# Optimization experiments

Measured on AMD Instinct MI355X. Metric: run time of the kernel, lower is better.

The kernel has to match this reference:

```python
import math
import jax, jax.numpy as jnp
import numpy as np

B, T, S, H, L, NH = 2, 512, 2048, 768, 32, 12
INTERMED = 4 * H


def _make_pe(max_len, hidden):
    position = np.arange(max_len)[:, None].astype(np.float32)
    div_term = np.exp(np.arange(0, hidden, 2).astype(np.float32) * (-math.log(10000.0) / hidden))
    pe = np.zeros((max_len, hidden), dtype=np.float32)
    pe[:, 0::2] = np.sin(position * div_term)
    pe[:, 1::2] = np.cos(position * div_term)
    return jnp.asarray(pe)


def setup_inputs() -> dict:
    key = jax.random.key(0)
    ks = jax.random.split(key, 10)
    token_reps = jax.random.normal(ks[0], (B, T, H), dtype=jnp.float32)
    starts = jax.random.randint(ks[1], (B, S), 0, T - L)
    lens = jax.random.randint(ks[2], (B, S), 1, L + 1)
    span_ids = jnp.stack([starts, starts + lens], axis=-1)  # (B,S,2)
    span_masks = jax.random.uniform(ks[3], (B, S)) > 0.2
    pe = _make_pe(T, H)
    dummy_query = jax.random.normal(ks[4], (H,), dtype=jnp.float32) * 0.02
    in_proj_w = jax.random.normal(ks[5], (3 * H, H), dtype=jnp.float32) * 0.02
    in_proj_b = jnp.zeros((3 * H,), jnp.float32)
    out_proj_w = jax.random.normal(ks[6], (H, H), dtype=jnp.float32) * 0.02
    out_proj_b = jnp.zeros((H,), jnp.float32)
    norm_g = jnp.ones((H,), jnp.float32)
    norm_b = jnp.zeros((H,), jnp.float32)
    ffn_w1 = jax.random.normal(ks[7], (INTERMED, H), dtype=jnp.float32) * (math.sqrt(2.0 / H))
    ffn_b1 = jnp.zeros((INTERMED,), jnp.float32)
    ffn_w2 = jax.random.normal(ks[8], (H, INTERMED), dtype=jnp.float32) * (math.sqrt(2.0 / INTERMED))
    ffn_b2 = jnp.zeros((H,), jnp.float32)
    return dict(token_reps=token_reps, span_ids=span_ids, span_masks=span_masks,
                pooling=0, pe=pe, dummy_query=dummy_query,
                in_proj_w=in_proj_w, in_proj_b=in_proj_b,
                out_proj_w=out_proj_w, out_proj_b=out_proj_b,
                norm_g=norm_g, norm_b=norm_b,
                ffn_w1=ffn_w1, ffn_b1=ffn_b1, ffn_w2=ffn_w2, ffn_b2=ffn_b2)


def _layernorm(x, g, b, eps=1e-5):
    mu = jnp.mean(x, axis=-1, keepdims=True)
    var = jnp.mean(jnp.square(x - mu), axis=-1, keepdims=True)
    return (x - mu) * jax.lax.rsqrt(var + eps) * g + b


def reference(token_reps, span_ids, span_masks, pooling, pe, dummy_query,
              in_proj_w, in_proj_b, out_proj_w, out_proj_b,
              norm_g, norm_b, ffn_w1, ffn_b1, ffn_w2, ffn_b2):
    b, t, h = token_reps.shape
    s = span_ids.shape[1]
    hd = h // NH
    # positional encoding over the sequence (dropout=0 / eval mode)
    x = token_reps + pe[:t]
    # ragged -> padded gather of span tokens
    starts = span_ids[..., 0]
    lens = (span_ids[..., 1] - starts) * span_masks.astype(span_ids.dtype)  # (B,S)
    ar = jnp.arange(L)
    pos = starts[..., None] + ar                     # (B,S,L)
    valid = ar[None, None, :] < lens[..., None]      # (B,S,L) True = real token
    idx = jnp.clip(pos, 0, t - 1)
    gathered = jax.vmap(lambda xb, ib: xb[ib])(x, idx)   # (B,S,L,H)
    gathered = gathered * valid[..., None]
    # guard fully-masked rows (masked-out / zero-len spans): keep one key valid,
    # output is zeroed at the end anyway (matches torch span_reps[~mask]=0)
    any_v = jnp.any(valid, axis=-1)
    valid = valid.at[..., 0].set(valid[..., 0] | ~any_v)
    # single-query multi-head attention (torch nn.MultiheadAttention math)
    Wq, Wk, Wv = jnp.split(in_proj_w, 3, axis=0)
    bq, bk, bv = jnp.split(in_proj_b, 3, axis=0)
    q = (dummy_query @ Wq.T + bq).reshape(NH, hd)                  # (NH,hd)
    k = (gathered @ Wk.T + bk).reshape(b, s, L, NH, hd)
    v = (gathered @ Wv.T + bv).reshape(b, s, L, NH, hd)
    scores = jnp.einsum('nd,bslnd->bsnl', q, k) / math.sqrt(hd)    # (B,S,NH,L)
    scores = jnp.where(valid[:, :, None, :], scores, -jnp.inf)
    attn = jax.nn.softmax(scores, axis=-1)
    ctx = jnp.einsum('bsnl,bslnd->bsnd', attn, v).reshape(b, s, h)
    attn_out = ctx @ out_proj_w.T + out_proj_b
    # residual + LayerNorm, FFN, residual + same LayerNorm
    x1 = _layernorm(attn_out + dummy_query, norm_g, norm_b)
    ffn = jax.nn.relu(x1 @ ffn_w1.T + ffn_b1) @ ffn_w2.T + ffn_b2
    out = _layernorm(ffn + x1, norm_g, norm_b)
    out = out * span_masks[..., None]
    return out
```

## Files before the change

kernel.cpp:

```cpp
#include <hip/hip_runtime.h>
#include <math.h>

static constexpr int B_  = 2;
static constexpr int T_  = 512;
static constexpr int S_  = 2048;
static constexpr int H_  = 768;
static constexpr int L_  = 32;
static constexpr int NH_ = 12;
static constexpr int HD_ = 64;
static constexpr int IM_ = 3072;

typedef __bf16 bf16x8 __attribute__((ext_vector_type(8)));
typedef float  f32x4  __attribute__((ext_vector_type(4)));

__device__ __forceinline__ float bf2f(unsigned short u) {
    return __uint_as_float(((unsigned)u) << 16);
}
__device__ __forceinline__ unsigned short f2bf(float f) {
    unsigned u = __float_as_uint(f);
    u += 0x7fffu + ((u >> 16) & 1u);
    return (unsigned short)(u >> 16);
}
__device__ __forceinline__ void gl_lds16(const void* g, void* l) {
    __builtin_amdgcn_global_load_lds((const __attribute__((address_space(1))) void*)g,
                                     (__attribute__((address_space(3))) void*)l, 16, 0, 0);
}

__global__ void k_q(const float* __restrict__ dq, const float* __restrict__ w,
                    const float* __restrict__ b, float* __restrict__ q,
                    const int* __restrict__ raw, int* __restrict__ mout) {
    int wv = threadIdx.x >> 6, lane = threadIdx.x & 63;
    int i = blockIdx.x * 4 + wv;
    const float* row = w + (size_t)i * H_;
    float acc = 0.f;
#pragma unroll
    for (int k = 0; k < 12; ++k) acc += dq[lane + 64 * k] * row[lane + 64 * k];
    for (int m = 32; m; m >>= 1) acc += __shfl_xor(acc, m, 64);
    if (lane == 0) q[i] = acc + b[i];
    if (blockIdx.x == 0) {
        __shared__ int bad;
        if (threadIdx.x == 0) bad = 0;
        __syncthreads();
        for (int t = threadIdx.x; t < 1024; t += 256) {
            int v = raw[t];
            if (v != 0 && v != 1) bad = 1;
        }
        __syncthreads();
        int byte_layout = bad;
        const unsigned char* rb = (const unsigned char*)raw;
        for (int t = threadIdx.x; t < B_ * S_; t += 256)
            mout[t] = byte_layout ? (int)rb[t] : raw[t];
    }
}

static constexpr int CWB = 2880;
__global__ void k_castw(const float* __restrict__ s0, const float* __restrict__ s1,
                        const float* __restrict__ s2, const float* __restrict__ s3,
                        unsigned short* __restrict__ d0, unsigned short* __restrict__ d1,
                        unsigned short* __restrict__ d2, unsigned short* __restrict__ d3,
                        const float* __restrict__ q, const float* __restrict__ wk,
                        float* __restrict__ wq) {
    if (blockIdx.x >= CWB) {
        int i = (blockIdx.x - CWB) * 256 + threadIdx.x;
        int n = i / H_, hh = i % H_;
        float acc = 0.f;
        for (int d = 0; d < HD_; ++d)
            acc += q[n * HD_ + d] * wk[(size_t)(H_ + n * HD_ + d) * H_ + hh];
        wq[i] = acc;
        return;
    }
    const long n0 = (long)H_ * H_, n2 = (long)IM_ * H_;
    long gid = (long)(blockIdx.x * 256 + threadIdx.x) * 8;
    const float* s; unsigned short* d; long off;
    if (gid < n0)                { s = s0; d = d0; off = gid; }
    else if (gid < 2 * n0)       { s = s1; d = d1; off = gid - n0; }
    else if (gid < 2 * n0 + n2)  { s = s2; d = d2; off = gid - 2 * n0; }
    else                         { s = s3; d = d3; off = gid - 2 * n0 - n2; }
    float4 f0 = *(const float4*)(s + off);
    float4 f1 = *(const float4*)(s + off + 4);
    uint4 o;
    o.x = (unsigned)f2bf(f0.x) | ((unsigned)f2bf(f0.y) << 16);
    o.y = (unsigned)f2bf(f0.z) | ((unsigned)f2bf(f0.w) << 16);
    o.z = (unsigned)f2bf(f1.x) | ((unsigned)f2bf(f1.y) << 16);
    o.w = (unsigned)f2bf(f1.z) | ((unsigned)f2bf(f1.w) << 16);
    *(uint4*)(d + off) = o;
}

__global__ void k_xstok(const float* __restrict__ tr, const float* __restrict__ pe,
                        const float* __restrict__ wq,
                        unsigned short* __restrict__ xbf, float* __restrict__ stok) {
    __shared__ float sx[H_];
    int bt = blockIdx.x, tid = threadIdx.x;
    const float* trow = tr + (size_t)bt * H_;
    const float* prow = pe + (size_t)(bt % T_) * H_;
    if (tid < 192) {
        int h0 = tid * 4;
        float4 a = *(const float4*)(trow + h0);
        float4 p = *(const float4*)(prow + h0);
        float v0 = a.x + p.x, v1 = a.y + p.y, v2 = a.z + p.z, v3 = a.w + p.w;
        sx[h0] = v0; sx[h0 + 1] = v1; sx[h0 + 2] = v2; sx[h0 + 3] = v3;
        uint2 o;
        o.x = (unsigned)f2bf(v0) | ((unsigned)f2bf(v1) << 16);
        o.y = (unsigned)f2bf(v2) | ((unsigned)f2bf(v3) << 16);
        *(uint2*)(xbf + (size_t)bt * H_ + h0) = o;
    }
    __syncthreads();
    int lane = tid & 63, w = tid >> 6;
    float xv[12];
#pragma unroll
    for (int k = 0; k < 12; ++k) xv[k] = sx[lane + 64 * k];
#pragma unroll
    for (int hh = 0; hh < 3; ++hh) {
        int n = w * 3 + hh;
        const float* wr = wq + (size_t)n * H_;
        float acc = 0.f;
#pragma unroll
        for (int k = 0; k < 12; ++k) acc += xv[k] * wr[lane + 64 * k];
        for (int m = 32; m; m >>= 1) acc += __shfl_xor(acc, m, 64);
        if (lane == 0) stok[bt * NH_ + n] = acc;
    }
}

__global__ void k_castv4(const unsigned short* __restrict__ p, size_t pstr,
                         unsigned short* __restrict__ dst, int n) {
    int i = (blockIdx.x * 256 + threadIdx.x) * 8;
    if (i >= n) return;
    float a[8] = {};
#pragma unroll
    for (int z = 0; z < 4; ++z) {
        uint4 u = *(const uint4*)(p + z * pstr + i);
        a[0] += bf2f((unsigned short)(u.x & 0xffff));
        a[1] += bf2f((unsigned short)(u.x >> 16));
        a[2] += bf2f((unsigned short)(u.y & 0xffff));
        a[3] += bf2f((unsigned short)(u.y >> 16));
        a[4] += bf2f((unsigned short)(u.z & 0xffff));
        a[5] += bf2f((unsigned short)(u.z >> 16));
        a[6] += bf2f((unsigned short)(u.w & 0xffff));
        a[7] += bf2f((unsigned short)(u.w >> 16));
    }
    uint4 o;
    o.x = (unsigned)f2bf(a[0]) | ((unsigned)f2bf(a[1]) << 16);
    o.y = (unsigned)f2bf(a[2]) | ((unsigned)f2bf(a[3]) << 16);
    o.z = (unsigned)f2bf(a[4]) | ((unsigned)f2bf(a[5]) << 16);
    o.w = (unsigned)f2bf(a[6]) | ((unsigned)f2bf(a[7]) << 16);
    *(uint4*)(dst + i) = o;
}

#define STG3(b_, k0e_) do {                                                   \
    unsigned short* _la = AsB + (b_) * 4096 + wid * 1024;                     \
    unsigned short* _lb = BsB + (b_) * 4096 + wid * 1024;                     \
    gl_lds16(agp + (k0e_), _la);                                              \
    gl_lds16(agp + (size_t)16 * K + (k0e_), _la + 512);                       \
    gl_lds16(bgp + (k0e_), _lb);                                              \
    gl_lds16(bgp + (size_t)16 * K + (k0e_), _lb + 512);                       \
} while (0)

template <bool RELU, bool SPLIT>
__device__ __forceinline__
void gemm_d3_body(const unsigned short* __restrict__ A, const unsigned short* __restrict__ W,
                  const float* __restrict__ bias, unsigned short* __restrict__ Cout,
                  int M, int N, int K, int kLen, int TX, int SP) {
    __shared__ unsigned short As[3][4096];
    __shared__ unsigned short Bs[3][4096];
    unsigned short* const AsB = &As[0][0];
    unsigned short* const BsB = &Bs[0][0];
    const int qx = blockIdx.x & 7, t = blockIdx.x >> 3;
    const int gi = t / TX, x = t - gi * TX;
    const int g = gi * 8 + qx;
    int y, z;
    if (SPLIT) { y = g / SP; z = g - y * SP; } else { y = g; z = 0; }
    const int bm = y * 128, bn = x * 128;
    const int kOff = z * kLen;

    const int tid = threadIdx.x, lane = tid & 63, wid = tid >> 6;
    const int wm = (wid >> 1) * 64, wn = (wid & 1) * 64;
    const int r16 = lane >> 2, c4 = lane & 3;
    const int swc = (c4 ^ ((r16 >> 1) & 3)) * 8;
    const unsigned short* agp = A + (size_t)(bm + wid * 32 + r16) * K + kOff + swc;
    const unsigned short* bgp = W + (size_t)(bn + wid * 32 + r16) * K + kOff + swc;

    f32x4 acc[4][4];
#pragma unroll
    for (int i = 0; i < 4; ++i)
#pragma unroll
        for (int j = 0; j < 4; ++j) acc[i][j] = f32x4{0.f, 0.f, 0.f, 0.f};

    const int mrow = lane & 15;
    const int q4 = lane >> 4;
    const int sw = (q4 ^ ((mrow >> 1) & 3)) * 8;
    const int NIT = kLen >> 5;

    STG3(0, 0);
    STG3(1, 1 << 5);
    int c0 = 0, c1 = 1, c2 = 2;
    for (int it = 0; it < NIT; ++it) {
        int nk = it + 2; if (nk > NIT - 1) nk = NIT - 1;
        STG3(c2, nk << 5);
        asm volatile("s_waitcnt vmcnt(8)" ::: "memory");
        __builtin_amdgcn_s_barrier();
        __builtin_amdgcn_sched_barrier(0);
        const unsigned short* Ac = AsB + c0 * 4096;
        const unsigned short* Bc = BsB + c0 * 4096;
        bf16x8 af[4], bfr[4];
#pragma unroll
        for (int i = 0; i < 4; ++i)
            af[i] = *(const bf16x8*)(Ac + (wm + i * 16 + mrow) * 32 + sw);
#pragma unroll
        for (int j = 0; j < 4; ++j)
            bfr[j] = *(const bf16x8*)(Bc + (wn + j * 16 + mrow) * 32 + sw);
        asm volatile("s_waitcnt lgkmcnt(0)" ::: "memory");
        __builtin_amdgcn_sched_barrier(0);
#pragma unroll
        for (int i = 0; i < 4; ++i)
#pragma unroll
            for (int j = 0; j < 4; ++j)
                acc[i][j] = __builtin_amdgcn_mfma_f32_16x16x32_bf16(af[i], bfr[j], acc[i][j], 0, 0, 0);
        __builtin_amdgcn_s_barrier();
        __builtin_amdgcn_sched_barrier(0);
        int tmp = c0; c0 = c1; c1 = c2; c2 = tmp;
    }
    asm volatile("s_waitcnt vmcnt(0)" ::: "memory");

    const bool addb = !SPLIT || z == 0;
    unsigned short* outp = SPLIT ? Cout + (size_t)z * M * N : Cout;
    const int lr = (lane >> 4) * 4, lc = lane & 15;
#pragma unroll
    for (int j = 0; j < 4; ++j) {
        int col = bn + wn + j * 16 + lc;
        float bv = addb ? bias[col] : 0.f;
#pragma unroll
        for (int i = 0; i < 4; ++i) {
            int row0 = bm + wm + i * 16 + lr;
#pragma unroll
            for (int r = 0; r < 4; ++r) {
                float v = acc[i][j][r] + bv;
                if (RELU) v = fmaxf(v, 0.f);
                outp[(size_t)(row0 + r) * N + col] = f2bf(v);
            }
        }
    }
}

__global__ __launch_bounds__(256)
void g3_vtok(const unsigned short* A, const unsigned short* W, const float* bias,
             unsigned short* Cout, int M, int N, int K, int kLen, int TX, int SP) {
    gemm_d3_body<false, true>(A, W, bias, Cout, M, N, K, kLen, TX, SP);
}
__global__ __launch_bounds__(256)
void g3_oproj(const unsigned short* A, const unsigned short* W, const float* bias,
              unsigned short* Cout, int M, int N, int K, int kLen, int TX, int SP) {
    gemm_d3_body<false, true>(A, W, bias, Cout, M, N, K, kLen, TX, SP);
}
__global__ __launch_bounds__(256)
void g3_ffn1(const unsigned short* A, const unsigned short* W, const float* bias,
             unsigned short* Cout, int M, int N, int K, int kLen, int TX, int SP) {
    gemm_d3_body<true, false>(A, W, bias, Cout, M, N, K, kLen, TX, SP);
}
__global__ __launch_bounds__(256)
void g3_ffn2(const unsigned short* A, const unsigned short* W, const float* bias,
             unsigned short* Cout, int M, int N, int K, int kLen, int TX, int SP) {
    gemm_d3_body<false, true>(A, W, bias, Cout, M, N, K, kLen, TX, SP);
}

__global__ void k_attn(const float* __restrict__ stok, const unsigned short* __restrict__ vtok,
                       const int* __restrict__ span_ids, const int* __restrict__ masks,
                       unsigned short* __restrict__ ctx) {
    int r = blockIdx.x, b = r / S_;
    unsigned short* out = ctx + (size_t)r * H_;
    int tid = threadIdx.x;
    __shared__ float w[NH_][L_];
    __shared__ int idxs[L_];
    __shared__ int s_len;
    if (tid == 0) {
        int m = masks[r];
        int st = span_ids[2 * r], en = span_ids[2 * r + 1];
        int len = m ? (en - st) : 0;
        len = len < 0 ? 0 : (len > L_ ? L_ : len);
        s_len = len;
    }
    __syncthreads();
    int len = s_len;
    if (len == 0) {
        for (int h2 = tid; h2 < H_ / 2; h2 += 256) ((unsigned*)out)[h2] = 0u;
        return;
    }
    if (tid < L_) {
        int p = span_ids[2 * r] + tid;
        idxs[tid] = p < 0 ? 0 : (p > T_ - 1 ? T_ - 1 : p);
    }
    __syncthreads();
    for (int i = tid; i < NH_ * L_; i += 256) {
        int n = i / L_, l = i % L_;
        w[n][l] = (l < len) ? stok[(size_t)(b * T_ + idxs[l]) * NH_ + n] * 0.125f : -INFINITY;
    }
    __syncthreads();
    if (tid < NH_) {
        float mx = -INFINITY;
        for (int l = 0; l < len; ++l) mx = fmaxf(mx, w[tid][l]);
        float sum = 0.f;
        for (int l = 0; l < len; ++l) { float e = __expf(w[tid][l] - mx); w[tid][l] = e; sum += e; }
        float inv = 1.f / sum;
        for (int l = 0; l < len; ++l) w[tid][l] *= inv;
    }
    __syncthreads();
    if (tid < 192) {
        int h0 = tid * 4, n = h0 >> 6;
        float a0 = 0.f, a1 = 0.f, a2 = 0.f, a3 = 0.f;
        for (int l = 0; l < len; ++l) {
            float wl = w[n][l];
            const unsigned short* vr = vtok + (size_t)(b * T_ + idxs[l]) * H_ + h0;
            uint2 u = *(const uint2*)vr;
            a0 += wl * bf2f((unsigned short)(u.x & 0xffff));
            a1 += wl * bf2f((unsigned short)(u.x >> 16));
            a2 += wl * bf2f((unsigned short)(u.y & 0xffff));
            a3 += wl * bf2f((unsigned short)(u.y >> 16));
        }
        uint2 o;
        o.x = (unsigned)f2bf(a0) | ((unsigned)f2bf(a1) << 16);
        o.y = (unsigned)f2bf(a2) | ((unsigned)f2bf(a3) << 16);
        *(uint2*)(out + h0) = o;
    }
}

template <bool RESROW, bool MASKOUT, int ZN>
__global__ void k_ln(const unsigned short* __restrict__ parts, size_t pstr,
                     const float* __restrict__ resf, const unsigned short* __restrict__ resb,
                     const float* __restrict__ g, const float* __restrict__ bt,
                     float* __restrict__ outf, unsigned short* __restrict__ outb,
                     const int* __restrict__ masks) {
    int r = blockIdx.x;
    int tid = threadIdx.x;
    float v[3];
    float lsum = 0.f;
#pragma unroll
    for (int i = 0; i < 3; ++i) {
        int h = tid + 256 * i;
        float s = RESROW ? bf2f(resb[(size_t)r * H_ + h]) : resf[h];
#pragma unroll
        for (int z = 0; z < ZN; ++z)
            s += bf2f(parts[z * pstr + (size_t)r * H_ + h]);
        v[i] = s;
        lsum += s;
    }
    __shared__ float sh[256];
    sh[tid] = lsum;
    __syncthreads();
    for (int st = 128; st > 0; st >>= 1) {
        if (tid < st) sh[tid] += sh[tid + st];
        __syncthreads();
    }
    float mean = sh[0] * (1.f / H_);
    __syncthreads();
    float lvar = 0.f;
#pragma unroll
    for (int i = 0; i < 3; ++i) { float d = v[i] - mean; lvar += d * d; }
    sh[tid] = lvar;
    __syncthreads();
    for (int st = 128; st > 0; st >>= 1) {
        if (tid < st) sh[tid] += sh[tid + st];
        __syncthreads();
    }
    float var = sh[0] * (1.f / H_);
    float scale = rsqrtf(var + 1e-5f);
    float mfac = 1.f;
    if (MASKOUT) mfac = masks[r] ? 1.f : 0.f;
#pragma unroll
    for (int i = 0; i < 3; ++i) {
        int h = tid + 256 * i;
        float o = ((v[i] - mean) * scale * g[h] + bt[h]) * mfac;
        if (MASKOUT) outf[(size_t)r * H_ + h] = o;
        else         outb[(size_t)r * H_ + h] = f2bf(o);
    }
}

extern "C" void kernel_launch(void* const* d_in, const int* in_sizes, int n_in,
                              void* d_out, int out_size, void* d_ws, size_t ws_size,
                              hipStream_t stream) {
    const float* token_reps = (const float*)d_in[0];
    const int*   span_ids   = (const int*)d_in[1];
    const int*   masks_raw  = (const int*)d_in[2];
    const float* pe   = (const float*)d_in[4];
    const float* dq   = (const float*)d_in[5];
    const float* in_w = (const float*)d_in[6];
    const float* in_b = (const float*)d_in[7];
    const float* ow   = (const float*)d_in[8];
    const float* ob   = (const float*)d_in[9];
    const float* g    = (const float*)d_in[10];
    const float* bt   = (const float*)d_in[11];
    const float* w1   = (const float*)d_in[12];
    const float* b1   = (const float*)d_in[13];
    const float* w2   = (const float*)d_in[14];
    const float* b2   = (const float*)d_in[15];

    const int BS = B_ * S_;
    const int BT = B_ * T_;

    float* fws   = (float*)d_ws;
    float* stok  = fws;
    float* qv    = stok + BT * NH_;
    float* wqeff = qv + H_;
    unsigned short* us = (unsigned short*)(wqeff + NH_ * H_);
    unsigned short* pbuf = us;
    unsigned short* xbf  = pbuf + (size_t)4 * BS * H_;
    unsigned short* vtok = xbf + (size_t)BT * H_;
    unsigned short* ctx  = vtok + (size_t)BT * H_;
    unsigned short* x1bf = ctx + (size_t)BS * H_;
    unsigned short* f1   = x1bf + (size_t)BS * H_;
    unsigned short* wvb  = f1 + (size_t)BS * IM_;
    unsigned short* owb  = wvb + H_ * H_;
    unsigned short* w1b  = owb + H_ * H_;
    unsigned short* w2b  = w1b + IM_ * H_;
    int* maskn = (int*)(w2b + H_ * IM_);

    k_q<<<H_ / 4, 256, 0, stream>>>(dq, in_w, in_b, qv, masks_raw, maskn);
    k_castw<<<CWB + 36, 256, 0, stream>>>(
        in_w + (size_t)2 * H_ * H_, ow, w1, w2, wvb, owb, w1b, w2b,
        qv, in_w, wqeff);
    k_xstok<<<BT, 256, 0, stream>>>(token_reps, pe, wqeff, xbf, stok);
    g3_vtok<<<192, 256, 0, stream>>>(
        xbf, wvb, in_b + 2 * H_, pbuf, BT, H_, H_, H_ / 4, 6, 4);
    k_castv4<<<(BT * H_ / 8 + 255) / 256, 256, 0, stream>>>(
        pbuf, (size_t)BT * H_, vtok, BT * H_);
    k_attn<<<BS, 256, 0, stream>>>(stok, vtok, span_ids, maskn, ctx);
    g3_oproj<<<384, 256, 0, stream>>>(
        ctx, owb, ob, pbuf, BS, H_, H_, H_ / 2, 6, 2);
    k_ln<false, false, 2><<<BS, 256, 0, stream>>>(
        pbuf, (size_t)BS * H_, dq, nullptr, g, bt, nullptr, x1bf, nullptr);
    g3_ffn1<<<768, 256, 0, stream>>>(
        x1bf, w1b, b1, f1, BS, IM_, H_, H_, 24, 1);
    g3_ffn2<<<384, 256, 0, stream>>>(
        f1, w2b, b2, pbuf, BS, H_, IM_, IM_ / 2, 6, 2);
    k_ln<true, true, 2><<<BS, 256, 0, stream>>>(
        pbuf, (size_t)BS * H_, nullptr, x1bf, g, bt, (float*)d_out, nullptr, maskn);
}
```

Before: 241.4 us.

## Fuse q projection into weight-cast kernel and split-K reduction into attention

```diff
diff --git a/kernel.cpp b/kernel.cpp
--- a/kernel.cpp
+++ b/kernel.cpp
@@ -26,51 +26,54 @@
                                      (__attribute__((address_space(3))) void*)l, 16, 0, 0);
 }
 
-__global__ void k_q(const float* __restrict__ dq, const float* __restrict__ w,
-                    const float* __restrict__ b, float* __restrict__ q,
-                    const int* __restrict__ raw, int* __restrict__ mout) {
-    int wv = threadIdx.x >> 6, lane = threadIdx.x & 63;
-    int i = blockIdx.x * 4 + wv;
-    const float* row = w + (size_t)i * H_;
-    float acc = 0.f;
-#pragma unroll
-    for (int k = 0; k < 12; ++k) acc += dq[lane + 64 * k] * row[lane + 64 * k];
-    for (int m = 32; m; m >>= 1) acc += __shfl_xor(acc, m, 64);
-    if (lane == 0) q[i] = acc + b[i];
-    if (blockIdx.x == 0) {
-        __shared__ int bad;
-        if (threadIdx.x == 0) bad = 0;
+static constexpr int CWB = 2880;
+__global__ void k_castw2(const float* __restrict__ s0, const float* __restrict__ s1,
+                         const float* __restrict__ s2, const float* __restrict__ s3,
+                         unsigned short* __restrict__ d0, unsigned short* __restrict__ d1,
+                         unsigned short* __restrict__ d2, unsigned short* __restrict__ d3,
+                         const float* __restrict__ dq, const float* __restrict__ in_w,
+                         const float* __restrict__ in_b, float* __restrict__ wq,
+                         const int* __restrict__ raw, int* __restrict__ mout) {
+    __shared__ float sq[64];
+    __shared__ int bad;
+    const int tid = threadIdx.x;
+    if (blockIdx.x >= CWB + 36) {
+        if (tid == 0) bad = 0;
         __syncthreads();
-        for (int t = threadIdx.x; t < 1024; t += 256) {
+        for (int t = tid; t < 1024; t += 256) {
             int v = raw[t];
             if (v != 0 && v != 1) bad = 1;
         }
         __syncthreads();
-        int byte_layout = bad;
+        int byl = bad;
         const unsigned char* rb = (const unsigned char*)raw;
-        for (int t = threadIdx.x; t < B_ * S_; t += 256)
-            mout[t] = byte_layout ? (int)rb[t] : raw[t];
-    }
-}
-
-static constexpr int CWB = 2880;
-__global__ void k_castw(const float* __restrict__ s0, const float* __restrict__ s1,
-                        const float* __restrict__ s2, const float* __restrict__ s3,
-                        unsigned short* __restrict__ d0, unsigned short* __restrict__ d1,
-                        unsigned short* __restrict__ d2, unsigned short* __restrict__ d3,
-                        const float* __restrict__ q, const float* __restrict__ wk,
-                        float* __restrict__ wq) {
+        int base = (blockIdx.x - (CWB + 36)) * 1024;
+#pragma unroll
+        for (int k = 0; k < 4; ++k) {
+            int t = base + k * 256 + tid;
+            mout[t] = byl ? (int)rb[t] : raw[t];
+        }
+        return;
+    }
     if (blockIdx.x >= CWB) {
-        int i = (blockIdx.x - CWB) * 256 + threadIdx.x;
-        int n = i / H_, hh = i % H_;
+        int wvb = blockIdx.x - CWB;
+        int n = wvb / 3, seg = wvb - n * 3;
+        if (tid < 64) {
+            const float* row = in_w + (size_t)(n * HD_ + tid) * H_;
+            float acc = 0.f;
+            for (int k = 0; k < H_; ++k) acc += dq[k] * row[k];
+            sq[tid] = acc + in_b[n * HD_ + tid];
+        }
+        __syncthreads();
+        int hh = seg * 256 + tid;
         float acc = 0.f;
         for (int d = 0; d < HD_; ++d)
-            acc += q[n * HD_ + d] * wk[(size_t)(H_ + n * HD_ + d) * H_ + hh];
-        wq[i] = acc;
+            acc += sq[d] * in_w[(size_t)(H_ + n * HD_ + d) * H_ + hh];
+        wq[n * H_ + hh] = acc;
         return;
     }
     const long n0 = (long)H_ * H_, n2 = (long)IM_ * H_;
-    long gid = (long)(blockIdx.x * 256 + threadIdx.x) * 8;
+    long gid = (long)(blockIdx.x * 256 + tid) * 8;
     const float* s; unsigned short* d; long off;
     if (gid < n0)                { s = s0; d = d0; off = gid; }
     else if (gid < 2 * n0)       { s = s1; d = d1; off = gid - n0; }
@@ -121,31 +124,6 @@
     }
 }
 
-__global__ void k_castv4(const unsigned short* __restrict__ p, size_t pstr,
-                         unsigned short* __restrict__ dst, int n) {
-    int i = (blockIdx.x * 256 + threadIdx.x) * 8;
-    if (i >= n) return;
-    float a[8] = {};
-#pragma unroll
-    for (int z = 0; z < 4; ++z) {
-        uint4 u = *(const uint4*)(p + z * pstr + i);
-        a[0] += bf2f((unsigned short)(u.x & 0xffff));
-        a[1] += bf2f((unsigned short)(u.x >> 16));
-        a[2] += bf2f((unsigned short)(u.y & 0xffff));
-        a[3] += bf2f((unsigned short)(u.y >> 16));
-        a[4] += bf2f((unsigned short)(u.z & 0xffff));
-        a[5] += bf2f((unsigned short)(u.z >> 16));
-        a[6] += bf2f((unsigned short)(u.w & 0xffff));
-        a[7] += bf2f((unsigned short)(u.w >> 16));
-    }
-    uint4 o;
-    o.x = (unsigned)f2bf(a[0]) | ((unsigned)f2bf(a[1]) << 16);
-    o.y = (unsigned)f2bf(a[2]) | ((unsigned)f2bf(a[3]) << 16);
-    o.z = (unsigned)f2bf(a[4]) | ((unsigned)f2bf(a[5]) << 16);
-    o.w = (unsigned)f2bf(a[6]) | ((unsigned)f2bf(a[7]) << 16);
-    *(uint4*)(dst + i) = o;
-}
-
 #define STG3(b_, k0e_) do {                                                   \
     unsigned short* _la = AsB + (b_) * 4096 + wid * 1024;                     \
     unsigned short* _lb = BsB + (b_) * 4096 + wid * 1024;                     \
@@ -262,9 +240,9 @@
     gemm_d3_body<false, true>(A, W, bias, Cout, M, N, K, kLen, TX, SP);
 }
 
-__global__ void k_attn(const float* __restrict__ stok, const unsigned short* __restrict__ vtok,
-                       const int* __restrict__ span_ids, const int* __restrict__ masks,
-                       unsigned short* __restrict__ ctx) {
+__global__ void k_attn4(const float* __restrict__ stok, const unsigned short* __restrict__ pbuf,
+                        size_t pstr, const int* __restrict__ span_ids,
+                        const int* __restrict__ masks, unsigned short* __restrict__ ctx) {
     int r = blockIdx.x, b = r / S_;
     unsigned short* out = ctx + (size_t)r * H_;
     int tid = threadIdx.x;
@@ -308,12 +286,17 @@
         float a0 = 0.f, a1 = 0.f, a2 = 0.f, a3 = 0.f;
         for (int l = 0; l < len; ++l) {
             float wl = w[n][l];
-            const unsigned short* vr = vtok + (size_t)(b * T_ + idxs[l]) * H_ + h0;
-            uint2 u = *(const uint2*)vr;
-            a0 += wl * bf2f((unsigned short)(u.x & 0xffff));
-            a1 += wl * bf2f((unsigned short)(u.x >> 16));
-            a2 += wl * bf2f((unsigned short)(u.y & 0xffff));
-            a3 += wl * bf2f((unsigned short)(u.y >> 16));
+            size_t ro = (size_t)(b * T_ + idxs[l]) * H_ + h0;
+            float s0 = 0.f, s1 = 0.f, s2 = 0.f, s3 = 0.f;
+#pragma unroll
+            for (int z = 0; z < 4; ++z) {
+                uint2 u = *(const uint2*)(pbuf + z * pstr + ro);
+                s0 += bf2f((unsigned short)(u.x & 0xffff));
+                s1 += bf2f((unsigned short)(u.x >> 16));
+                s2 += bf2f((unsigned short)(u.y & 0xffff));
+                s3 += bf2f((unsigned short)(u.y >> 16));
+            }
+            a0 += wl * s0; a1 += wl * s1; a2 += wl * s2; a3 += wl * s3;
         }
         uint2 o;
         o.x = (unsigned)f2bf(a0) | ((unsigned)f2bf(a1) << 16);
@@ -412,16 +395,13 @@
     unsigned short* w2b  = w1b + IM_ * H_;
     int* maskn = (int*)(w2b + H_ * IM_);
 
-    k_q<<<H_ / 4, 256, 0, stream>>>(dq, in_w, in_b, qv, masks_raw, maskn);
-    k_castw<<<CWB + 36, 256, 0, stream>>>(
+    k_castw2<<<CWB + 40, 256, 0, stream>>>(
         in_w + (size_t)2 * H_ * H_, ow, w1, w2, wvb, owb, w1b, w2b,
-        qv, in_w, wqeff);
+        dq, in_w, in_b, wqeff, masks_raw, maskn);
     k_xstok<<<BT, 256, 0, stream>>>(token_reps, pe, wqeff, xbf, stok);
     g3_vtok<<<192, 256, 0, stream>>>(
         xbf, wvb, in_b + 2 * H_, pbuf, BT, H_, H_, H_ / 4, 6, 4);
-    k_castv4<<<(BT * H_ / 8 + 255) / 256, 256, 0, stream>>>(
-        pbuf, (size_t)BT * H_, vtok, BT * H_);
-    k_attn<<<BS, 256, 0, stream>>>(stok, vtok, span_ids, maskn, ctx);
+    k_attn4<<<BS, 256, 0, stream>>>(stok, pbuf, (size_t)BT * H_, span_ids, maskn, ctx);
     g3_oproj<<<384, 256, 0, stream>>>(
         ctx, owb, ob, pbuf, BS, H_, H_, H_ / 2, 6, 2);
     k_ln<false, false, 2><<<BS, 256, 0, stream>>>(
```

Result: slower. 261.1 us (+8.2%).

## Split-K the FFN1 GEMM and raise split factor for oproj and FFN2

Applied to the files above, without the earlier changes.

```diff
diff --git a/kernel.cpp b/kernel.cpp
--- a/kernel.cpp
+++ b/kernel.cpp
@@ -146,6 +146,26 @@
     *(uint4*)(dst + i) = o;
 }
 
+__global__ void k_sumrelu(unsigned short* __restrict__ f1,
+                          const unsigned short* __restrict__ pext, int n) {
+    int i = (blockIdx.x * 256 + threadIdx.x) * 8;
+    if (i >= n) return;
+    uint4 u0 = *(const uint4*)(f1 + i);
+    uint4 u1 = *(const uint4*)(pext + i);
+    uint4 o;
+    unsigned* pu0 = (unsigned*)&u0;
+    unsigned* pu1 = (unsigned*)&u1;
+    unsigned* po  = (unsigned*)&o;
+#pragma unroll
+    for (int k = 0; k < 4; ++k) {
+        float a0 = bf2f((unsigned short)(pu0[k] & 0xffff)) + bf2f((unsigned short)(pu1[k] & 0xffff));
+        float a1 = bf2f((unsigned short)(pu0[k] >> 16))    + bf2f((unsigned short)(pu1[k] >> 16));
+        a0 = fmaxf(a0, 0.f); a1 = fmaxf(a1, 0.f);
+        po[k] = (unsigned)f2bf(a0) | ((unsigned)f2bf(a1) << 16);
+    }
+    *(uint4*)(f1 + i) = o;
+}
+
 #define STG3(b_, k0e_) do {                                                   \
     unsigned short* _la = AsB + (b_) * 4096 + wid * 1024;                     \
     unsigned short* _lb = BsB + (b_) * 4096 + wid * 1024;                     \
@@ -155,10 +175,11 @@
     gl_lds16(bgp + (size_t)16 * K + (k0e_), _lb + 512);                       \
 } while (0)
 
-template <bool RELU, bool SPLIT>
+template <bool RELU, bool SPLIT, bool DUAL>
 __device__ __forceinline__
 void gemm_d3_body(const unsigned short* __restrict__ A, const unsigned short* __restrict__ W,
                   const float* __restrict__ bias, unsigned short* __restrict__ Cout,
+                  unsigned short* __restrict__ Cout2,
                   int M, int N, int K, int kLen, int TX, int SP) {
     __shared__ unsigned short As[3][4096];
     __shared__ unsigned short Bs[3][4096];
@@ -222,7 +243,10 @@
     asm volatile("s_waitcnt vmcnt(0)" ::: "memory");
 
     const bool addb = !SPLIT || z == 0;
-    unsigned short* outp = SPLIT ? Cout + (size_t)z * M * N : Cout;
+    unsigned short* outp;
+    if (DUAL)       outp = (z == 0) ? Cout : Cout2;
+    else if (SPLIT) outp = Cout + (size_t)z * M * N;
+    else            outp = Cout;
     const int lr = (lane >> 4) * 4, lc = lane & 15;
 #pragma unroll
     for (int j = 0; j < 4; ++j) {
@@ -244,22 +268,23 @@
 __global__ __launch_bounds__(256)
 void g3_vtok(const unsigned short* A, const unsigned short* W, const float* bias,
              unsigned short* Cout, int M, int N, int K, int kLen, int TX, int SP) {
-    gemm_d3_body<false, true>(A, W, bias, Cout, M, N, K, kLen, TX, SP);
+    gemm_d3_body<false, true, false>(A, W, bias, Cout, nullptr, M, N, K, kLen, TX, SP);
 }
 __global__ __launch_bounds__(256)
 void g3_oproj(const unsigned short* A, const unsigned short* W, const float* bias,
               unsigned short* Cout, int M, int N, int K, int kLen, int TX, int SP) {
-    gemm_d3_body<false, true>(A, W, bias, Cout, M, N, K, kLen, TX, SP);
+    gemm_d3_body<false, true, false>(A, W, bias, Cout, nullptr, M, N, K, kLen, TX, SP);
 }
 __global__ __launch_bounds__(256)
-void g3_ffn1(const unsigned short* A, const unsigned short* W, const float* bias,
-             unsigned short* Cout, int M, int N, int K, int kLen, int TX, int SP) {
-    gemm_d3_body<true, false>(A, W, bias, Cout, M, N, K, kLen, TX, SP);
+void g3_ffn1s(const unsigned short* A, const unsigned short* W, const float* bias,
+              unsigned short* Cout, unsigned short* Cout2,
+              int M, int N, int K, int kLen, int TX, int SP) {
+    gemm_d3_body<false, true, true>(A, W, bias, Cout, Cout2, M, N, K, kLen, TX, SP);
 }
 __global__ __launch_bounds__(256)
 void g3_ffn2(const unsigned short* A, const unsigned short* W, const float* bias,
              unsigned short* Cout, int M, int N, int K, int kLen, int TX, int SP) {
-    gemm_d3_body<false, true>(A, W, bias, Cout, M, N, K, kLen, TX, SP);
+    gemm_d3_body<false, true, false>(A, W, bias, Cout, nullptr, M, N, K, kLen, TX, SP);
 }
 
 __global__ void k_attn(const float* __restrict__ stok, const unsigned short* __restrict__ vtok,
@@ -422,14 +447,16 @@
     k_castv4<<<(BT * H_ / 8 + 255) / 256, 256, 0, stream>>>(
         pbuf, (size_t)BT * H_, vtok, BT * H_);
     k_attn<<<BS, 256, 0, stream>>>(stok, vtok, span_ids, maskn, ctx);
-    g3_oproj<<<384, 256, 0, stream>>>(
-        ctx, owb, ob, pbuf, BS, H_, H_, H_ / 2, 6, 2);
-    k_ln<false, false, 2><<<BS, 256, 0, stream>>>(
+    g3_oproj<<<768, 256, 0, stream>>>(
+        ctx, owb, ob, pbuf, BS, H_, H_, H_ / 4, 6, 4);
+    k_ln<false, false, 4><<<BS, 256, 0, stream>>>(
         pbuf, (size_t)BS * H_, dq, nullptr, g, bt, nullptr, x1bf, nullptr);
-    g3_ffn1<<<768, 256, 0, stream>>>(
-        x1bf, w1b, b1, f1, BS, IM_, H_, H_, 24, 1);
-    g3_ffn2<<<384, 256, 0, stream>>>(
-        f1, w2b, b2, pbuf, BS, H_, IM_, IM_ / 2, 6, 2);
-    k_ln<true, true, 2><<<BS, 256, 0, stream>>>(
+    g3_ffn1s<<<1536, 256, 0, stream>>>(
+        x1bf, w1b, b1, f1, pbuf, BS, IM_, H_, H_ / 2, 24, 2);
+    k_sumrelu<<<(BS * IM_ / 8 + 255) / 256, 256, 0, stream>>>(
+        f1, pbuf, BS * IM_);
+    g3_ffn2<<<768, 256, 0, stream>>>(
+        f1, w2b, b2, pbuf, BS, H_, IM_, IM_ / 4, 6, 4);
+    k_ln<true, true, 4><<<BS, 256, 0, stream>>>(
         pbuf, (size_t)BS * H_, nullptr, x1bf, g, bt, (float*)d_out, nullptr, maskn);
 }
```

Result: slower. 261.1 us (+8.1%).

## Replace FFN1 GEMM with 512-thread 256x128-tile triple-buffered kernel

Applied to the files above, without the earlier changes.

```diff
diff --git a/kernel.cpp b/kernel.cpp
--- a/kernel.cpp
+++ b/kernel.cpp
@@ -252,14 +252,97 @@
     gemm_d3_body<false, true>(A, W, bias, Cout, M, N, K, kLen, TX, SP);
 }
 __global__ __launch_bounds__(256)
-void g3_ffn1(const unsigned short* A, const unsigned short* W, const float* bias,
-             unsigned short* Cout, int M, int N, int K, int kLen, int TX, int SP) {
-    gemm_d3_body<true, false>(A, W, bias, Cout, M, N, K, kLen, TX, SP);
-}
-__global__ __launch_bounds__(256)
 void g3_ffn2(const unsigned short* A, const unsigned short* W, const float* bias,
              unsigned short* Cout, int M, int N, int K, int kLen, int TX, int SP) {
     gemm_d3_body<false, true>(A, W, bias, Cout, M, N, K, kLen, TX, SP);
+}
+
+__global__ __launch_bounds__(512)
+void g8_ffn1(const unsigned short* __restrict__ A, const unsigned short* __restrict__ W,
+             const float* __restrict__ bias, unsigned short* __restrict__ Cout,
+             int M, int N, int K, int kLen, int TX) {
+    __shared__ unsigned short As[3][8192];
+    __shared__ unsigned short Bs[3][4096];
+    unsigned short* const AsB = &As[0][0];
+    unsigned short* const BsB = &Bs[0][0];
+    const int qx = blockIdx.x & 7, t = blockIdx.x >> 3;
+    const int gi = t / TX, x = t - gi * TX;
+    const int y = gi * 8 + qx;
+    const int bm = y * 256, bn = x * 128;
+
+    const int tid = threadIdx.x, lane = tid & 63, wid = tid >> 6;
+    const int wm = (wid >> 1) * 64, wn = (wid & 1) * 64;
+    const int r16 = lane >> 2, c4 = lane & 3;
+    const int swc = (c4 ^ ((r16 >> 1) & 3)) * 8;
+    const unsigned short* agp = A + (size_t)(bm + wid * 32 + r16) * K + swc;
+    const unsigned short* bgp = W + (size_t)(bn + wid * 16 + r16) * K + swc;
+
+#define STG8(b_, k0e_) do {                                                   \
+    unsigned short* _la = AsB + (b_) * 8192 + wid * 1024;                     \
+    unsigned short* _lb = BsB + (b_) * 4096 + wid * 512;                      \
+    gl_lds16(agp + (k0e_), _la);                                              \
+    gl_lds16(agp + (size_t)16 * K + (k0e_), _la + 512);                       \
+    gl_lds16(bgp + (k0e_), _lb);                                              \
+} while (0)
+
+    f32x4 acc[4][4];
+#pragma unroll
+    for (int i = 0; i < 4; ++i)
+#pragma unroll
+        for (int j = 0; j < 4; ++j) acc[i][j] = f32x4{0.f, 0.f, 0.f, 0.f};
+
+    const int mrow = lane & 15;
+    const int q4 = lane >> 4;
+    const int sw = (q4 ^ ((mrow >> 1) & 3)) * 8;
+    const int NIT = kLen >> 5;
+
+    STG8(0, 0);
+    STG8(1, 1 << 5);
+    int c0 = 0, c1 = 1, c2 = 2;
+    for (int it = 0; it < NIT; ++it) {
+        int nk = it + 2; if (nk > NIT - 1) nk = NIT - 1;
+        STG8(c2, nk << 5);
+        asm volatile("s_waitcnt vmcnt(6)" ::: "memory");
+        __builtin_amdgcn_s_barrier();
+        __builtin_amdgcn_sched_barrier(0);
+        const unsigned short* Ac = AsB + c0 * 8192;
+        const unsigned short* Bc = BsB + c0 * 4096;
+        bf16x8 af[4], bfr[4];
+#pragma unroll
+        for (int i = 0; i < 4; ++i)
+            af[i] = *(const bf16x8*)(Ac + (wm + i * 16 + mrow) * 32 + sw);
+#pragma unroll
+        for (int j = 0; j < 4; ++j)
+            bfr[j] = *(const bf16x8*)(Bc + (wn + j * 16 + mrow) * 32 + sw);
+        asm volatile("s_waitcnt lgkmcnt(0)" ::: "memory");
+        __builtin_amdgcn_sched_barrier(0);
+#pragma unroll
+        for (int i = 0; i < 4; ++i)
+#pragma unroll
+            for (int j = 0; j < 4; ++j)
+                acc[i][j] = __builtin_amdgcn_mfma_f32_16x16x32_bf16(af[i], bfr[j], acc[i][j], 0, 0, 0);
+        __builtin_amdgcn_s_barrier();
+        __builtin_amdgcn_sched_barrier(0);
+        int tmp = c0; c0 = c1; c1 = c2; c2 = tmp;
+    }
+    asm volatile("s_waitcnt vmcnt(0)" ::: "memory");
+
+    const int lr = (lane >> 4) * 4, lc = lane & 15;
+#pragma unroll
+    for (int j = 0; j < 4; ++j) {
+        int col = bn + wn + j * 16 + lc;
+        float bv = bias[col];
+#pragma unroll
+        for (int i = 0; i < 4; ++i) {
+            int row0 = bm + wm + i * 16 + lr;
+#pragma unroll
+            for (int r = 0; r < 4; ++r) {
+                float v = fmaxf(acc[i][j][r] + bv, 0.f);
+                Cout[(size_t)(row0 + r) * N + col] = f2bf(v);
+            }
+        }
+    }
+#undef STG8
 }
 
 __global__ void k_attn(const float* __restrict__ stok, const unsigned short* __restrict__ vtok,
@@ -426,8 +509,8 @@
         ctx, owb, ob, pbuf, BS, H_, H_, H_ / 2, 6, 2);
     k_ln<false, false, 2><<<BS, 256, 0, stream>>>(
         pbuf, (size_t)BS * H_, dq, nullptr, g, bt, nullptr, x1bf, nullptr);
-    g3_ffn1<<<768, 256, 0, stream>>>(
-        x1bf, w1b, b1, f1, BS, IM_, H_, H_, 24, 1);
+    g8_ffn1<<<384, 512, 0, stream>>>(
+        x1bf, w1b, b1, f1, BS, IM_, H_, H_, 24);
     g3_ffn2<<<384, 256, 0, stream>>>(
         f1, w2b, b2, pbuf, BS, H_, IM_, IM_ / 2, 6, 2);
     k_ln<true, true, 2><<<BS, 256, 0, stream>>>(
```

Result: no change. 242.7 us (+0.5%).
